# Kernel tuning notes

Measured on AMD Instinct MI355X. Metric: run time of the kernel, lower is better.

Reference implementation:

```python
import jax, jax.numpy as jnp
import numpy as np

N_NODES = 50000
N_EDGES = 800000
HIDDEN = 128
N_TYPES = 4
TIME_STEPS = [2]  # one layer, 2 propagation steps; residuals = {}


def setup_inputs() -> dict:
    key = jax.random.key(0)
    ks = jax.random.split(key, 8)
    std = HIDDEN ** (-0.5)
    states = jax.random.normal(ks[0], (N_NODES, HIDDEN), dtype=jnp.float32)
    etype = jax.random.randint(ks[1], (N_EDGES,), 0, N_TYPES, dtype=jnp.int32)
    src = jax.random.randint(ks[2], (N_EDGES,), 0, N_NODES, dtype=jnp.int32)
    tgt = jax.random.randint(ks[3], (N_EDGES,), 0, N_NODES, dtype=jnp.int32)
    edges = jnp.stack([etype, src, tgt], axis=1)  # [E, 3]: (type, source, target)
    type_weights = std * jax.random.normal(ks[4], (N_TYPES, HIDDEN, HIDDEN), dtype=jnp.float32)
    type_biases = std * jax.random.normal(ks[5], (N_TYPES, HIDDEN), dtype=jnp.float32)
    # Keras GRUCell (reset_after=True): kernel [H,3H], recurrent_kernel [H,3H], bias [2,3H]
    gru_kernel = std * jax.random.normal(ks[6], (HIDDEN, 3 * HIDDEN), dtype=jnp.float32)
    k7, k8 = jax.random.split(ks[7])
    gru_rec_kernel = std * jax.random.normal(k7, (HIDDEN, 3 * HIDDEN), dtype=jnp.float32)
    gru_bias = std * jax.random.normal(k8, (2, 3 * HIDDEN), dtype=jnp.float32)
    return {"states": states, "edges": edges, "type_weights": type_weights,
            "type_biases": type_biases, "gru_kernel": gru_kernel,
            "gru_rec_kernel": gru_rec_kernel, "gru_bias": gru_bias}


def _gru_cell(x, h, kernel, rec_kernel, bias):
    # Keras GRUCell with reset_after=True, tanh / sigmoid activations
    mx = x @ kernel + bias[0]          # [N, 3H]
    mh = h @ rec_kernel + bias[1]      # [N, 3H]
    xz, xr, xh = jnp.split(mx, 3, axis=-1)
    rz, rr, rh = jnp.split(mh, 3, axis=-1)
    z = jax.nn.sigmoid(xz + rz)
    r = jax.nn.sigmoid(xr + rr)
    hh = jnp.tanh(xh + r * rh)
    return z * h + (1.0 - z) * hh


def _propagate(h, etype, src, tgt, type_weights, type_biases, kernel, rec_kernel, bias):
    n_nodes = h.shape[0]
    xs = h[src]  # [E, H] gather of source states
    msg_e = jnp.zeros_like(xs)
    for t in range(N_TYPES):  # small fixed loop over edge types
        mask = (etype == t).astype(h.dtype)[:, None]
        msg_e = msg_e + mask * (xs @ type_weights[t] + type_biases[t])
    messages = jax.ops.segment_sum(msg_e, tgt, num_segments=n_nodes)  # scatter-add
    return _gru_cell(messages, h, kernel, rec_kernel, bias)


def reference(states, edges, type_weights, type_biases, gru_kernel, gru_rec_kernel, gru_bias):
    etype, src, tgt = edges[:, 0], edges[:, 1], edges[:, 2]
    h = states
    for steps in TIME_STEPS:  # single layer here (residuals empty)
        for _ in range(steps):
            h = _propagate(h, etype, src, tgt, type_weights, type_biases,
                           gru_kernel, gru_rec_kernel, gru_bias)
    return h
```

## Files before the change

kernel.cpp:

```cpp
#include <hip/hip_runtime.h>
#include <stdint.h>

namespace {
constexpr int kNodes = 50000;
constexpr int kEdges = 800000;
constexpr int kHid   = 128;
constexpr int kScanBlocks = (kNodes + 255) / 256;
constexpr int kBlocks32 = (kNodes + 31) / 32;

constexpr size_t oCounts    = 0;
constexpr size_t oCursor    = 200704;
constexpr size_t oBlockSums = 401408;
constexpr size_t oBpack     = 402432;
constexpr size_t oPacked    = 1057792;
constexpr size_t oMsg      = 4257792;
constexpr size_t oY         = 29857792;
constexpr size_t kWsNeeded   = oY + 51200000;
constexpr size_t kWsFallback = oY;

constexpr size_t bKhi = 0,      bKlo = 98304,  bRhi = 196608,
                 bRlo = 294912, bWhi = 393216, bWlo = 524288;
}

typedef __attribute__((ext_vector_type(8))) short short8;
typedef __attribute__((ext_vector_type(4))) float f32x4;

union ABFrag { short8 v; uint16_t u[8]; uint4 q; };

__device__ __forceinline__ uint16_t f2bf(float x) {
  uint32_t u = __float_as_uint(x);
  return (uint16_t)((u + 0x7FFFu + ((u >> 16) & 1u)) >> 16);
}
__device__ __forceinline__ float bf2f(uint16_t h) {
  return __uint_as_float(((uint32_t)h) << 16);
}

__device__ __forceinline__ float fast_rcp(float x) {
#if __has_builtin(__builtin_amdgcn_rcpf)
  return __builtin_amdgcn_rcpf(x);
#else
  return 1.f / x;
#endif
}
__device__ __forceinline__ float fast_exp2(float x) {
#if __has_builtin(__builtin_amdgcn_exp2f)
  return __builtin_amdgcn_exp2f(x);
#else
  return exp2f(x);
#endif
}
__device__ __forceinline__ float sigf(float x) {
  return fast_rcp(1.f + fast_exp2(-1.4426950408889634f * x));
}
__device__ __forceinline__ float tanh_fast(float x) {
  x = fminf(fmaxf(x, -10.f), 10.f);
  const float t = fast_exp2(2.8853900817779268f * x);
  return (t - 1.f) * fast_rcp(t + 1.f);
}

__device__ __forceinline__ int swz_pi(int p) {
  return (p & 64) | ((p & 3) << 4) | ((p >> 2) & 15);
}


__global__ __launch_bounds__(256) void count_kernel(const int* __restrict__ edges,
                                                    int* __restrict__ counts) {
  int e = blockIdx.x * 256 + threadIdx.x;
  if (e < kEdges) atomicAdd(&counts[edges[e * 3 + 2]], 1);
}

__global__ __launch_bounds__(256) void scan1_kernel(const int* __restrict__ counts,
                                                    int* __restrict__ cursor,
                                                    int* __restrict__ blocksums) {
  __shared__ int sd[256];
  const int t = threadIdx.x;
  const int i = blockIdx.x * 256 + t;
  int v = (i < kNodes) ? counts[i] : 0;
  sd[t] = v;
  __syncthreads();
  for (int off = 1; off < 256; off <<= 1) {
    int x = (t >= off) ? sd[t - off] : 0;
    __syncthreads();
    sd[t] += x;
    __syncthreads();
  }
  if (i < kNodes) cursor[i] = sd[t] - v;
  if (t == 255) blocksums[blockIdx.x] = sd[255];
}

__global__ __launch_bounds__(256) void scan2_kernel(int* __restrict__ blocksums) {
  __shared__ int sd[256];
  const int t = threadIdx.x;
  int v = (t < kScanBlocks) ? blocksums[t] : 0;
  sd[t] = v;
  __syncthreads();
  for (int off = 1; off < 256; off <<= 1) {
    int x = (t >= off) ? sd[t - off] : 0;
    __syncthreads();
    sd[t] += x;
    __syncthreads();
  }
  if (t < kScanBlocks) blocksums[t] = sd[t] - v;
}

__global__ __launch_bounds__(256) void scan3_kernel(int* __restrict__ cursor,
                                                    const int* __restrict__ blocksums) {
  const int i = blockIdx.x * 256 + threadIdx.x;
  if (i < kNodes) cursor[i] += blocksums[blockIdx.x];
}

__global__ __launch_bounds__(256) void fill_kernel(const int* __restrict__ edges,
                                                   int* __restrict__ cursor,
                                                   unsigned* __restrict__ packed) {
  int e = blockIdx.x * 256 + threadIdx.x;
  if (e < kEdges) {
    const int et  = edges[e * 3 + 0];
    const int src = edges[e * 3 + 1];
    const int tgt = edges[e * 3 + 2];
    const int pos = atomicAdd(&cursor[tgt], 1);
    packed[pos] = (unsigned)(src * 4 + et);
  }
}

__global__ __launch_bounds__(256) void pack_b_kernel(
    const float* __restrict__ K,
    const float* __restrict__ R,
    const float* __restrict__ W,
    uint16_t* __restrict__ bp) {
  const int idx = blockIdx.x * 256 + threadIdx.x;
  uint16_t* khi = bp + bKhi / 2;
  uint16_t* klo = bp + bKlo / 2;
  uint16_t* rhi = bp + bRhi / 2;
  uint16_t* rlo = bp + bRlo / 2;
  uint16_t* whi = bp + bWhi / 2;
  uint16_t* wlo = bp + bWlo / 2;
  if (idx < 128 * 384) {
    const int k = idx / 384, c = idx % 384;
    const int ksrc = swz_pi(k);
    const int kt = k >> 5, quad = (k >> 3) & 3, j = k & 7;
    const int nt = c >> 4, ln = (c & 15) | (quad << 4);
    const size_t o = ((size_t)(kt * 24 + nt) * 64 + ln) * 8 + j;
    const float kv = K[ksrc * 384 + c];
    const float rv = R[k * 384 + c];
    const uint16_t kh = f2bf(kv), rh = f2bf(rv);
    khi[o] = kh; klo[o] = f2bf(kv - bf2f(kh));
    rhi[o] = rh; rlo[o] = f2bf(rv - bf2f(rh));
  } else if (idx < 128 * 384 + 128 * 512) {
    const int i2 = idx - 128 * 384;
    const int k = i2 / 512, c = i2 % 512;
    const int t = c >> 7, cc = c & 127;
    const float wv = W[((size_t)t * 128 + k) * 128 + cc];
    const int kt = k >> 5, quad = (k >> 3) & 3, j = k & 7;
    const int nt = c >> 4, ln = (c & 15) | (quad << 4);
    const size_t o = ((size_t)(kt * 32 + nt) * 64 + ln) * 8 + j;
    const uint16_t wh = f2bf(wv);
    whi[o] = wh; wlo[o] = f2bf(wv - bf2f(wh));
  }
}

__device__ __forceinline__ void split8(const float* p, ABFrag& hi, ABFrag& lo) {
  const float4 a0 = *(const float4*)p;
  const float4 a1 = *(const float4*)(p + 4);
  const float v[8] = {a0.x, a0.y, a0.z, a0.w, a1.x, a1.y, a1.z, a1.w};
#pragma unroll
  for (int j = 0; j < 8; ++j) {
    const uint16_t t = f2bf(v[j]);
    hi.u[j] = t; lo.u[j] = f2bf(v[j] - bf2f(t));
  }
}
__device__ __forceinline__ void conv8(const float* p, ABFrag& hi) {
  const float4 a0 = *(const float4*)p;
  const float4 a1 = *(const float4*)(p + 4);
  const float v[8] = {a0.x, a0.y, a0.z, a0.w, a1.x, a1.y, a1.z, a1.w};
#pragma unroll
  for (int j = 0; j < 8; ++j) hi.u[j] = f2bf(v[j]);
}

__global__ __launch_bounds__(64, 4) void transform_mfma(
    const float* __restrict__ h,
    const uint16_t* __restrict__ bp,
    const float* __restrict__ TB,
    uint16_t* __restrict__ y16) {
  const int lane = threadIdx.x;
  const int w = blockIdx.x & 3;
  const int col16 = lane & 15, quad = lane >> 4;
  const int node0 = (blockIdx.x >> 2) * 32;

  const uint4* __restrict__ Whi = (const uint4*)(bp + bWhi / 2);
  const uint4* __restrict__ Wlo = (const uint4*)(bp + bWlo / 2);

  bool mok[2];
#pragma unroll
  for (int m = 0; m < 2; ++m) mok[m] = (node0 + m * 16) < kNodes;

  f32x4 acc[8][2];
#pragma unroll
  for (int nt = 0; nt < 8; ++nt)
#pragma unroll
    for (int m = 0; m < 2; ++m) acc[nt][m] = (f32x4){0.f, 0.f, 0.f, 0.f};

  const float* hrow = h + (size_t)(node0 + col16) * kHid + quad * 8;

#pragma unroll
  for (int kt = 0; kt < 4; ++kt) {
    ABFrag ah[2], al[2];
#pragma unroll
    for (int m = 0; m < 2; ++m) {
      if (mok[m]) {
        split8(hrow + (size_t)m * 16 * kHid + kt * 32, ah[m], al[m]);
      } else {
        ah[m].q = make_uint4(0, 0, 0, 0); al[m].q = ah[m].q;
      }
    }
#pragma unroll
    for (int nt = 0; nt < 8; ++nt) {
      ABFrag bh, bl;
      bh.q = Whi[(size_t)(kt * 32 + w * 8 + nt) * 64 + lane];
      bl.q = Wlo[(size_t)(kt * 32 + w * 8 + nt) * 64 + lane];
#pragma unroll
      for (int m = 0; m < 2; ++m) {
        f32x4 c = acc[nt][m];
        c = __builtin_amdgcn_mfma_f32_16x16x32_bf16(ah[m].v, bh.v, c, 0, 0, 0);
        c = __builtin_amdgcn_mfma_f32_16x16x32_bf16(ah[m].v, bl.v, c, 0, 0, 0);
        c = __builtin_amdgcn_mfma_f32_16x16x32_bf16(al[m].v, bh.v, c, 0, 0, 0);
        acc[nt][m] = c;
      }
    }
  }

#pragma unroll
  for (int g = 0; g < 2; ++g) {
    float bias[4];
#pragma unroll
    for (int s = 0; s < 4; ++s) bias[s] = TB[w * 128 + (g * 4 + s) * 16 + col16];
#pragma unroll
    for (int m = 0; m < 2; ++m) {
      if (!mok[m]) continue;
#pragma unroll
      for (int r = 0; r < 4; ++r) {
        const int node = node0 + m * 16 + quad * 4 + r;
        const uint32_t lo = (uint32_t)f2bf(acc[g * 4 + 0][m][r] + bias[0]) |
                            ((uint32_t)f2bf(acc[g * 4 + 1][m][r] + bias[1]) << 16);
        const uint32_t hi = (uint32_t)f2bf(acc[g * 4 + 2][m][r] + bias[2]) |
                            ((uint32_t)f2bf(acc[g * 4 + 3][m][r] + bias[3]) << 16);
        *(uint2*)&y16[(size_t)node * 512 + w * 128 + g * 64 + col16 * 4] =
            make_uint2(lo, hi);
      }
    }
  }
}

__global__ __launch_bounds__(256) void gather_kernel(
    const uint32_t* __restrict__ y2,
    const uint32_t* __restrict__ packed,
    const int* __restrict__ rowend,
    const int* __restrict__ counts,
    uint32_t* __restrict__ msg2) {
  const int tid = threadIdx.x;
  const int lane = tid & 63;
  const int v = blockIdx.x * 4 + (tid >> 6);
  const int cnt = counts[v];
  const int s0 = rowend[v] - cnt;
  float a0 = 0.f, a1 = 0.f;
  int e = 0;
  for (; e + 8 <= cnt; e += 8) {
    uint32_t p[8], u[8];
#pragma unroll
    for (int i = 0; i < 8; ++i) p[i] = packed[s0 + e + i];
#pragma unroll
    for (int i = 0; i < 8; ++i) u[i] = y2[(size_t)p[i] * 64 + lane];
#pragma unroll
    for (int i = 0; i < 8; ++i) {
      a0 += __uint_as_float(u[i] << 16);
      a1 += __uint_as_float(u[i] & 0xFFFF0000u);
    }
  }
  for (; e < cnt; ++e) {
    const uint32_t p = packed[s0 + e];
    const uint32_t u = y2[(size_t)p * 64 + lane];
    a0 += __uint_as_float(u << 16);
    a1 += __uint_as_float(u & 0xFFFF0000u);
  }
  msg2[(size_t)v * 64 + lane] = (uint32_t)f2bf(a0) | ((uint32_t)f2bf(a1) << 16);
}

__global__ __launch_bounds__(256, 3) void gru_mfma(
    const uint16_t* __restrict__ msg16,
    const float* __restrict__ hin,
    const uint16_t* __restrict__ bp,
    const float* __restrict__ gb,
    float* __restrict__ hout) {
  const int tid = threadIdx.x;
  const int w = tid >> 6;
  const int lane = tid & 63;
  const int col16 = lane & 15, quad = lane >> 4;
  const int node0 = blockIdx.x * 32;

  const uint4* __restrict__ Khi = (const uint4*)(bp + bKhi / 2);
  const uint4* __restrict__ Klo = (const uint4*)(bp + bKlo / 2);
  const uint4* __restrict__ Rhi = (const uint4*)(bp + bRhi / 2);
  const uint4* __restrict__ Rlo = (const uint4*)(bp + bRlo / 2);

  bool mok[2];
#pragma unroll
  for (int m = 0; m < 2; ++m) mok[m] = (node0 + m * 16) < kNodes;

  f32x4 aZ[2][2], aR[2][2], aX[2][2], aH[2][2];
#pragma unroll
  for (int i = 0; i < 2; ++i)
#pragma unroll
    for (int m = 0; m < 2; ++m) {
      aZ[i][m] = (f32x4){0.f, 0.f, 0.f, 0.f};
      aR[i][m] = aZ[i][m]; aX[i][m] = aZ[i][m]; aH[i][m] = aZ[i][m];
    }

  const uint16_t* mrow = msg16 + (size_t)(node0 + col16) * kHid + quad * 8;
  const float* hrow = hin + (size_t)(node0 + col16) * kHid + quad * 8;

#pragma unroll
  for (int kt = 0; kt < 4; ++kt) {
    ABFrag mh[2], hh[2];
#pragma unroll
    for (int m = 0; m < 2; ++m) {
      if (mok[m]) {
        mh[m].q = *(const uint4*)(mrow + (size_t)m * 16 * kHid + kt * 32);
        conv8(hrow + (size_t)m * 16 * kHid + kt * 32, hh[m]);
      } else {
        mh[m].q = make_uint4(0, 0, 0, 0); hh[m].q = mh[m].q;
      }
    }
#pragma unroll
    for (int lnt = 0; lnt < 2; ++lnt) {
      const int ntc = w * 2 + lnt;
      const size_t oz = (size_t)(kt * 24 + ntc) * 64 + lane;
      const size_t orr = (size_t)(kt * 24 + 8 + ntc) * 64 + lane;
      const size_t oh = (size_t)(kt * 24 + 16 + ntc) * 64 + lane;
      {
        ABFrag kzh, kzl, rzh, rzl, krh, krl, rrh, rrl;
        kzh.q = Khi[oz]; kzl.q = Klo[oz]; rzh.q = Rhi[oz]; rzl.q = Rlo[oz];
        krh.q = Khi[orr]; krl.q = Klo[orr]; rrh.q = Rhi[orr]; rrl.q = Rlo[orr];
#pragma unroll
        for (int m = 0; m < 2; ++m) {
          f32x4 z = aZ[lnt][m];
          z = __builtin_amdgcn_mfma_f32_16x16x32_bf16(mh[m].v, kzh.v, z, 0, 0, 0);
          z = __builtin_amdgcn_mfma_f32_16x16x32_bf16(mh[m].v, kzl.v, z, 0, 0, 0);
          z = __builtin_amdgcn_mfma_f32_16x16x32_bf16(hh[m].v, rzh.v, z, 0, 0, 0);
          z = __builtin_amdgcn_mfma_f32_16x16x32_bf16(hh[m].v, rzl.v, z, 0, 0, 0);
          aZ[lnt][m] = z;
          f32x4 r = aR[lnt][m];
          r = __builtin_amdgcn_mfma_f32_16x16x32_bf16(mh[m].v, krh.v, r, 0, 0, 0);
          r = __builtin_amdgcn_mfma_f32_16x16x32_bf16(mh[m].v, krl.v, r, 0, 0, 0);
          r = __builtin_amdgcn_mfma_f32_16x16x32_bf16(hh[m].v, rrh.v, r, 0, 0, 0);
          r = __builtin_amdgcn_mfma_f32_16x16x32_bf16(hh[m].v, rrl.v, r, 0, 0, 0);
          aR[lnt][m] = r;
        }
      }
      {
        ABFrag khh, khl, rhh, rhl;
        khh.q = Khi[oh]; khl.q = Klo[oh]; rhh.q = Rhi[oh]; rhl.q = Rlo[oh];
#pragma unroll
        for (int m = 0; m < 2; ++m) {
          f32x4 x = aX[lnt][m];
          x = __builtin_amdgcn_mfma_f32_16x16x32_bf16(mh[m].v, khh.v, x, 0, 0, 0);
          x = __builtin_amdgcn_mfma_f32_16x16x32_bf16(mh[m].v, khl.v, x, 0, 0, 0);
          aX[lnt][m] = x;
          f32x4 y = aH[lnt][m];
          y = __builtin_amdgcn_mfma_f32_16x16x32_bf16(hh[m].v, rhh.v, y, 0, 0, 0);
          y = __builtin_amdgcn_mfma_f32_16x16x32_bf16(hh[m].v, rhl.v, y, 0, 0, 0);
          aH[lnt][m] = y;
        }
      }
    }
  }

  __syncthreads();

#pragma unroll
  for (int lnt = 0; lnt < 2; ++lnt) {
    const int c = (w * 2 + lnt) * 16 + col16;
    const float bz = gb[c] + gb[384 + c];
    const float br = gb[128 + c] + gb[512 + c];
    const float bx = gb[256 + c];
    const float bh = gb[640 + c];
#pragma unroll
    for (int m = 0; m < 2; ++m) {
      if (!mok[m]) continue;
#pragma unroll
      for (int r = 0; r < 4; ++r) {
        const int node = node0 + m * 16 + quad * 4 + r;
        const float hp = hin[(size_t)node * kHid + c];
        const float z = sigf(aZ[lnt][m][r] + bz);
        const float rr = sigf(aR[lnt][m][r] + br);
        const float hh = tanh_fast(aX[lnt][m][r] + bx + rr * (aH[lnt][m][r] + bh));
        hout[(size_t)node * kHid + c] = z * hp + (1.f - z) * hh;
      }
    }
  }
}


__global__ __launch_bounds__(256, 2) void message_fb_kernel(
    const float* __restrict__ hin,
    const unsigned* __restrict__ packed,
    const int* __restrict__ rowend,
    const int* __restrict__ counts,
    const float* __restrict__ W,
    const float* __restrict__ TB,
    float* __restrict__ msg) {
  __shared__ float S[32 * 512];
  __shared__ int D[32][4];
  const int tid = threadIdx.x;
  {
    const int g = tid >> 7;
    const int j = tid & 127;
    for (int i = 0; i < 16; ++i) {
      const int nl = g * 16 + i;
      const int v = blockIdx.x * 32 + nl;
      if (v >= kNodes) break;
      const int cnt = counts[v];
      const int s0 = rowend[v] - cnt;
      float a0 = 0.f, a1 = 0.f, a2 = 0.f, a3 = 0.f;
      int d0 = 0, d1 = 0, d2 = 0, d3 = 0;
      for (int e = 0; e < cnt; ++e) {
        const unsigned p = packed[s0 + e];
        const int src = (int)(p >> 2);
        const int t = (int)(p & 3u);
        const float val = hin[(size_t)src * kHid + j];
        a0 += (t == 0) ? val : 0.f;
        a1 += (t == 1) ? val : 0.f;
        a2 += (t == 2) ? val : 0.f;
        a3 += (t == 3) ? val : 0.f;
        d0 += (t == 0); d1 += (t == 1); d2 += (t == 2); d3 += (t == 3);
      }
      float* Sn = &S[nl * 512];
      Sn[j] = a0; Sn[128 + j] = a1; Sn[256 + j] = a2; Sn[384 + j] = a3;
      if (j == 0) { D[nl][0] = d0; D[nl][1] = d1; D[nl][2] = d2; D[nl][3] = d3; }
    }
  }
  __syncthreads();

  const int lane = tid & 31;
  const int jj = lane * 4;
  const int n0 = (tid >> 5) * 4;
  float acc[4][4] = {};
  const float4* __restrict__ W4 = (const float4*)W;
  for (int tk = 0; tk < 512; tk += 4) {
    const float4 w0 = W4[(size_t)(tk + 0) * 32 + lane];
    const float4 w1 = W4[(size_t)(tk + 1) * 32 + lane];
    const float4 w2 = W4[(size_t)(tk + 2) * 32 + lane];
    const float4 w3 = W4[(size_t)(tk + 3) * 32 + lane];
#pragma unroll
    for (int n = 0; n < 4; ++n) {
      const float4 s = *(const float4*)&S[(n0 + n) * 512 + tk];
      acc[n][0] += s.x * w0.x + s.y * w1.x + s.z * w2.x + s.w * w3.x;
      acc[n][1] += s.x * w0.y + s.y * w1.y + s.z * w2.y + s.w * w3.y;
      acc[n][2] += s.x * w0.z + s.y * w1.z + s.z * w2.z + s.w * w3.z;
      acc[n][3] += s.x * w0.w + s.y * w1.w + s.z * w2.w + s.w * w3.w;
    }
  }
  const float4 B0 = *(const float4*)&TB[0 * 128 + jj];
  const float4 B1 = *(const float4*)&TB[1 * 128 + jj];
  const float4 B2 = *(const float4*)&TB[2 * 128 + jj];
  const float4 B3 = *(const float4*)&TB[3 * 128 + jj];
#pragma unroll
  for (int n = 0; n < 4; ++n) {
    const int v = blockIdx.x * 32 + n0 + n;
    if (v < kNodes) {
      float4 o;
      const float d0 = (float)D[n0 + n][0], d1 = (float)D[n0 + n][1];
      const float d2 = (float)D[n0 + n][2], d3 = (float)D[n0 + n][3];
      o.x = acc[n][0] + d0 * B0.x + d1 * B1.x + d2 * B2.x + d3 * B3.x;
      o.y = acc[n][1] + d0 * B0.y + d1 * B1.y + d2 * B2.y + d3 * B3.y;
      o.z = acc[n][2] + d0 * B0.z + d1 * B1.z + d2 * B2.z + d3 * B3.z;
      o.w = acc[n][3] + d0 * B0.w + d1 * B1.w + d2 * B2.w + d3 * B3.w;
      *(float4*)&msg[(size_t)v * kHid + jj] = o;
    }
  }
}

__global__ __launch_bounds__(256, 2) void gru_fb_kernel(
    const float* __restrict__ msg,
    const float* __restrict__ hin,
    const float* __restrict__ K,
    const float* __restrict__ R,
    const float* __restrict__ gb,
    float* __restrict__ hout) {
  __shared__ float At[2][16][68];
  __shared__ float Bt[2][16][384];
  const int tid = threadIdx.x;
  const int node0 = blockIdx.x * 64;
  const int cg = tid >> 4;
  const int ng = tid & 15;

  float accZ[4][8] = {}, accR[4][8] = {}, accXH[4][8] = {}, accRH[4][8] = {};
  const float4* __restrict__ K4 = (const float4*)K;
  const float4* __restrict__ R4 = (const float4*)R;
  const int sn = tid >> 2;
  const int sj = tid & 3;

  for (int k0 = 0; k0 < 128; k0 += 16) {
    __syncthreads();
    {
      float4 vm = make_float4(0.f, 0.f, 0.f, 0.f);
      float4 vh = vm;
      const int node = node0 + sn;
      if (node < kNodes) {
        vm = *(const float4*)&msg[(size_t)node * kHid + k0 + sj * 4];
        vh = *(const float4*)&hin[(size_t)node * kHid + k0 + sj * 4];
      }
      At[0][sj * 4 + 0][sn] = vm.x; At[0][sj * 4 + 1][sn] = vm.y;
      At[0][sj * 4 + 2][sn] = vm.z; At[0][sj * 4 + 3][sn] = vm.w;
      At[1][sj * 4 + 0][sn] = vh.x; At[1][sj * 4 + 1][sn] = vh.y;
      At[1][sj * 4 + 2][sn] = vh.z; At[1][sj * 4 + 3][sn] = vh.w;
    }
#pragma unroll
    for (int i = 0; i < 6; ++i) {
      const int idx = tid + i * 256;
      const int row = idx / 96;
      const int c4 = idx - row * 96;
      *(float4*)&Bt[0][row][c4 * 4] = K4[(size_t)(k0 + row) * 96 + c4];
      *(float4*)&Bt[1][row][c4 * 4] = R4[(size_t)(k0 + row) * 96 + c4];
    }
    __syncthreads();

    for (int kk = 0; kk < 16; ++kk) {
      const float4 am4 = *(const float4*)&At[0][kk][ng * 4];
      const float4 ah4 = *(const float4*)&At[1][kk][ng * 4];
      const float am[4] = {am4.x, am4.y, am4.z, am4.w};
      const float ah[4] = {ah4.x, ah4.y, ah4.z, ah4.w};
      const int cb = cg * 8;
#pragma unroll
      for (int gset = 0; gset < 3; ++gset) {
        const int off = gset * 128 + cb;
        const float4 k0v = *(const float4*)&Bt[0][kk][off];
        const float4 k1v = *(const float4*)&Bt[0][kk][off + 4];
        const float4 r0v = *(const float4*)&Bt[1][kk][off];
        const float4 r1v = *(const float4*)&Bt[1][kk][off + 4];
        const float bk[8] = {k0v.x, k0v.y, k0v.z, k0v.w, k1v.x, k1v.y, k1v.z, k1v.w};
        const float br[8] = {r0v.x, r0v.y, r0v.z, r0v.w, r1v.x, r1v.y, r1v.z, r1v.w};
        if (gset == 0) {
#pragma unroll
          for (int n = 0; n < 4; ++n)
#pragma unroll
            for (int c = 0; c < 8; ++c) accZ[n][c] += am[n] * bk[c] + ah[n] * br[c];
        } else if (gset == 1) {
#pragma unroll
          for (int n = 0; n < 4; ++n)
#pragma unroll
            for (int c = 0; c < 8; ++c) accR[n][c] += am[n] * bk[c] + ah[n] * br[c];
        } else {
#pragma unroll
          for (int n = 0; n < 4; ++n)
#pragma unroll
            for (int c = 0; c < 8; ++c) {
              accXH[n][c] += am[n] * bk[c];
              accRH[n][c] += ah[n] * br[c];
            }
        }
      }
    }
  }

  const int cb = cg * 8;
#pragma unroll
  for (int n = 0; n < 4; ++n) {
    const int node = node0 + ng * 4 + n;
    if (node >= kNodes) continue;
    float o[8];
#pragma unroll
    for (int c = 0; c < 8; ++c) {
      const float z = sigf(accZ[n][c] + gb[cb + c] + gb[384 + cb + c]);
      const float r = sigf(accR[n][c] + gb[128 + cb + c] + gb[512 + cb + c]);
      const float hh = tanh_fast(accXH[n][c] + gb[256 + cb + c] +
                                 r * (accRH[n][c] + gb[640 + cb + c]));
      const float hp = hin[(size_t)node * kHid + cb + c];
      o[c] = z * hp + (1.f - z) * hh;
    }
    *(float4*)&hout[(size_t)node * kHid + cb]     = make_float4(o[0], o[1], o[2], o[3]);
    *(float4*)&hout[(size_t)node * kHid + cb + 4] = make_float4(o[4], o[5], o[6], o[7]);
  }
}

extern "C" void kernel_launch(void* const* d_in, const int* in_sizes, int n_in,
                              void* d_out, int out_size, void* d_ws, size_t ws_size,
                              hipStream_t stream) {
  const float* states = (const float*)d_in[0];
  const int*   edges  = (const int*)d_in[1];
  const float* W      = (const float*)d_in[2];
  const float* TB     = (const float*)d_in[3];
  const float* K      = (const float*)d_in[4];
  const float* R      = (const float*)d_in[5];
  const float* gb     = (const float*)d_in[6];
  float* out = (float*)d_out;

  if (ws_size < kWsFallback) return;

  char* ws = (char*)d_ws;
  int*      counts  = (int*)(ws + oCounts);
  int*      cursor  = (int*)(ws + oCursor);
  int*      bsums   = (int*)(ws + oBlockSums);
  uint16_t* bpack   = (uint16_t*)(ws + oBpack);
  unsigned* packed  = (unsigned*)(ws + oPacked);
  float*    msgf    = (float*)(ws + oMsg);
  uint16_t* msg16   = (uint16_t*)(ws + oMsg);
  uint32_t* msg2    = (uint32_t*)(ws + oMsg);
  uint16_t* y16     = (uint16_t*)(ws + oY);
  uint32_t* y2      = (uint32_t*)(ws + oY);

  hipMemsetAsync(counts, 0, 200704, stream);
  count_kernel<<<kEdges / 256, 256, 0, stream>>>(edges, counts);
  scan1_kernel<<<kScanBlocks, 256, 0, stream>>>(counts, cursor, bsums);
  scan2_kernel<<<1, 256, 0, stream>>>(bsums);
  scan3_kernel<<<kScanBlocks, 256, 0, stream>>>(cursor, bsums);
  fill_kernel<<<kEdges / 256, 256, 0, stream>>>(edges, cursor, packed);

  if (ws_size >= kWsNeeded) {
    pack_b_kernel<<<448, 256, 0, stream>>>(K, R, W, bpack);
    const int ga_blocks = kNodes / 4;
    const int tf_blocks = kBlocks32 * 4;
    transform_mfma<<<tf_blocks, 64, 0, stream>>>(states, bpack, TB, y16);
    gather_kernel<<<ga_blocks, 256, 0, stream>>>(y2, packed, cursor, counts, msg2);
    gru_mfma<<<kBlocks32, 256, 0, stream>>>(msg16, states, bpack, gb, out);
    transform_mfma<<<tf_blocks, 64, 0, stream>>>(out, bpack, TB, y16);
    gather_kernel<<<ga_blocks, 256, 0, stream>>>(y2, packed, cursor, counts, msg2);
    gru_mfma<<<kBlocks32, 256, 0, stream>>>(msg16, out, bpack, gb, out);
  } else {
    const int msg_blocks = (kNodes + 31) / 32;
    const int gru_blocks = (kNodes + 63) / 64;
    message_fb_kernel<<<msg_blocks, 256, 0, stream>>>(states, packed, cursor,
                                                      counts, W, TB, msgf);
    gru_fb_kernel<<<gru_blocks, 256, 0, stream>>>(msgf, states, K, R, gb, out);
    message_fb_kernel<<<msg_blocks, 256, 0, stream>>>(out, packed, cursor,
                                                      counts, W, TB, msgf);
    gru_fb_kernel<<<gru_blocks, 256, 0, stream>>>(msgf, out, K, R, gb, out);
  }
}
```

Baseline: 420.2 us.

## Stage packed weight fragments through double-buffered LDS in transform and GRU kernels

```diff
diff --git a/kernel.cpp b/kernel.cpp
--- a/kernel.cpp
+++ b/kernel.cpp
@@ -6,7 +6,7 @@
 constexpr int kEdges = 800000;
 constexpr int kHid   = 128;
 constexpr int kScanBlocks = (kNodes + 255) / 256;
-constexpr int kBlocks32 = (kNodes + 31) / 32;
+constexpr int kBlocks64 = (kNodes + 63) / 64;
 
 constexpr size_t oCounts    = 0;
 constexpr size_t oCursor    = 200704;
@@ -60,6 +60,12 @@
 
 __device__ __forceinline__ int swz_pi(int p) {
   return (p & 64) | ((p & 3) << 4) | ((p >> 2) & 15);
+}
+
+__device__ __forceinline__ void gload_lds16(const void* g, void* l) {
+  __builtin_amdgcn_global_load_lds(
+      (const __attribute__((address_space(1))) unsigned int*)g,
+      (__attribute__((address_space(3))) unsigned int*)l, 16, 0, 0);
 }
 
 
@@ -158,9 +164,7 @@
   }
 }
 
-__device__ __forceinline__ void split8(const float* p, ABFrag& hi, ABFrag& lo) {
-  const float4 a0 = *(const float4*)p;
-  const float4 a1 = *(const float4*)(p + 4);
+__device__ __forceinline__ void split8v(float4 a0, float4 a1, ABFrag& hi, ABFrag& lo) {
   const float v[8] = {a0.x, a0.y, a0.z, a0.w, a1.x, a1.y, a1.z, a1.w};
 #pragma unroll
   for (int j = 0; j < 8; ++j) {
@@ -168,30 +172,31 @@
     hi.u[j] = t; lo.u[j] = f2bf(v[j] - bf2f(t));
   }
 }
-__device__ __forceinline__ void conv8(const float* p, ABFrag& hi) {
-  const float4 a0 = *(const float4*)p;
-  const float4 a1 = *(const float4*)(p + 4);
+__device__ __forceinline__ void conv8v(float4 a0, float4 a1, ABFrag& hi) {
   const float v[8] = {a0.x, a0.y, a0.z, a0.w, a1.x, a1.y, a1.z, a1.w};
 #pragma unroll
   for (int j = 0; j < 8; ++j) hi.u[j] = f2bf(v[j]);
 }
 
-__global__ __launch_bounds__(64, 4) void transform_mfma(
+__global__ __launch_bounds__(512, 2) void transform_mfma(
     const float* __restrict__ h,
     const uint16_t* __restrict__ bp,
     const float* __restrict__ TB,
     uint16_t* __restrict__ y16) {
-  const int lane = threadIdx.x;
-  const int w = blockIdx.x & 3;
+  __shared__ uint4 smem[2][32][64];
+  const int tid = threadIdx.x;
+  const int W = tid >> 6;
+  const int tw = W & 3;
+  const int hf = W >> 2;
+  const int lane = tid & 63;
   const int col16 = lane & 15, quad = lane >> 4;
-  const int node0 = (blockIdx.x >> 2) * 32;
-
-  const uint4* __restrict__ Whi = (const uint4*)(bp + bWhi / 2);
-  const uint4* __restrict__ Wlo = (const uint4*)(bp + bWlo / 2);
+  const int node0 = blockIdx.x * 64 + hf * 32;
+  const char* wb = (const char*)bp + bWhi;
+  const int r0 = W * 4;
 
   bool mok[2];
-#pragma unroll
-  for (int m = 0; m < 2; ++m) mok[m] = (node0 + m * 16) < kNodes;
+  mok[0] = node0 < kNodes;
+  mok[1] = node0 + 16 < kNodes;
 
   f32x4 acc[8][2];
 #pragma unroll
@@ -202,28 +207,68 @@
   const float* hrow = h + (size_t)(node0 + col16) * kHid + quad * 8;
 
 #pragma unroll
+  for (int i = 0; i < 4; ++i) {
+    const int r = r0 + i;
+    const int tbl = r >> 4, w_ = (r >> 2) & 3, j = r & 3;
+    gload_lds16(wb + (size_t)tbl * 131072 + (size_t)(w_ * 8 + j) * 1024 + lane * 16,
+                &smem[0][r][0]);
+  }
+
+  ABFrag ah[2], al[2];
+#pragma unroll
   for (int kt = 0; kt < 4; ++kt) {
-    ABFrag ah[2], al[2];
-#pragma unroll
-    for (int m = 0; m < 2; ++m) {
-      if (mok[m]) {
-        split8(hrow + (size_t)m * 16 * kHid + kt * 32, ah[m], al[m]);
-      } else {
-        ah[m].q = make_uint4(0, 0, 0, 0); al[m].q = ah[m].q;
-      }
-    }
-#pragma unroll
-    for (int nt = 0; nt < 8; ++nt) {
-      ABFrag bh, bl;
-      bh.q = Whi[(size_t)(kt * 32 + w * 8 + nt) * 64 + lane];
-      bl.q = Wlo[(size_t)(kt * 32 + w * 8 + nt) * 64 + lane];
-#pragma unroll
-      for (int m = 0; m < 2; ++m) {
-        f32x4 c = acc[nt][m];
-        c = __builtin_amdgcn_mfma_f32_16x16x32_bf16(ah[m].v, bh.v, c, 0, 0, 0);
-        c = __builtin_amdgcn_mfma_f32_16x16x32_bf16(ah[m].v, bl.v, c, 0, 0, 0);
-        c = __builtin_amdgcn_mfma_f32_16x16x32_bf16(al[m].v, bh.v, c, 0, 0, 0);
-        acc[nt][m] = c;
+    float4 araw[2][2];
+#pragma unroll
+    for (int g = 0; g < 2; ++g) {
+      const int c = kt * 2 + g;
+      asm volatile("s_waitcnt vmcnt(0)" ::: "memory");
+      __builtin_amdgcn_s_barrier();
+      asm volatile("" ::: "memory");
+      if (g == 0) {
+#pragma unroll
+        for (int m = 0; m < 2; ++m) {
+          if (mok[m]) {
+            araw[m][0] = *(const float4*)(hrow + (size_t)m * 16 * kHid + kt * 32);
+            araw[m][1] = *(const float4*)(hrow + (size_t)m * 16 * kHid + kt * 32 + 4);
+          } else {
+            araw[m][0] = make_float4(0.f, 0.f, 0.f, 0.f);
+            araw[m][1] = araw[m][0];
+          }
+        }
+      }
+      asm volatile("" ::: "memory");
+      if (c + 1 < 8) {
+        const int nk = (c + 1) >> 1, ng = (c + 1) & 1;
+#pragma unroll
+        for (int i = 0; i < 4; ++i) {
+          const int r = r0 + i;
+          const int tbl = r >> 4, w_ = (r >> 2) & 3, j = r & 3;
+          gload_lds16(wb + (size_t)tbl * 131072 +
+                          (size_t)(nk * 32 + w_ * 8 + ng * 4 + j) * 1024 + lane * 16,
+                      &smem[(c + 1) & 1][r][0]);
+        }
+      }
+      asm volatile("" ::: "memory");
+      if (g == 0) {
+#pragma unroll
+        for (int m = 0; m < 2; ++m) split8v(araw[m][0], araw[m][1], ah[m], al[m]);
+      }
+      const int b = c & 1;
+#pragma unroll
+      for (int jj = 0; jj < 4; ++jj) {
+        ABFrag bh, bl;
+        bh.q = smem[b][tw * 4 + jj][lane];
+        bl.q = smem[b][16 + tw * 4 + jj][lane];
+        __builtin_amdgcn_s_setprio(1);
+#pragma unroll
+        for (int m = 0; m < 2; ++m) {
+          f32x4 cc = acc[g * 4 + jj][m];
+          cc = __builtin_amdgcn_mfma_f32_16x16x32_bf16(ah[m].v, bh.v, cc, 0, 0, 0);
+          cc = __builtin_amdgcn_mfma_f32_16x16x32_bf16(ah[m].v, bl.v, cc, 0, 0, 0);
+          cc = __builtin_amdgcn_mfma_f32_16x16x32_bf16(al[m].v, bh.v, cc, 0, 0, 0);
+          acc[g * 4 + jj][m] = cc;
+        }
+        __builtin_amdgcn_s_setprio(0);
       }
     }
   }
@@ -232,7 +277,7 @@
   for (int g = 0; g < 2; ++g) {
     float bias[4];
 #pragma unroll
-    for (int s = 0; s < 4; ++s) bias[s] = TB[w * 128 + (g * 4 + s) * 16 + col16];
+    for (int s = 0; s < 4; ++s) bias[s] = TB[tw * 128 + (g * 4 + s) * 16 + col16];
 #pragma unroll
     for (int m = 0; m < 2; ++m) {
       if (!mok[m]) continue;
@@ -243,7 +288,7 @@
                             ((uint32_t)f2bf(acc[g * 4 + 1][m][r] + bias[1]) << 16);
         const uint32_t hi = (uint32_t)f2bf(acc[g * 4 + 2][m][r] + bias[2]) |
                             ((uint32_t)f2bf(acc[g * 4 + 3][m][r] + bias[3]) << 16);
-        *(uint2*)&y16[(size_t)node * 512 + w * 128 + g * 64 + col16 * 4] =
+        *(uint2*)&y16[(size_t)node * 512 + tw * 128 + g * 64 + col16 * 4] =
             make_uint2(lo, hi);
       }
     }
@@ -284,26 +329,26 @@
   msg2[(size_t)v * 64 + lane] = (uint32_t)f2bf(a0) | ((uint32_t)f2bf(a1) << 16);
 }
 
-__global__ __launch_bounds__(256, 3) void gru_mfma(
+__global__ __launch_bounds__(512, 2) void gru_mfma(
     const uint16_t* __restrict__ msg16,
     const float* __restrict__ hin,
     const uint16_t* __restrict__ bp,
     const float* __restrict__ gb,
     float* __restrict__ hout) {
+  __shared__ uint4 smem[2][32][64];
   const int tid = threadIdx.x;
-  const int w = tid >> 6;
+  const int W = tid >> 6;
+  const int cg = W & 3;
+  const int hf = W >> 2;
   const int lane = tid & 63;
   const int col16 = lane & 15, quad = lane >> 4;
-  const int node0 = blockIdx.x * 32;
-
-  const uint4* __restrict__ Khi = (const uint4*)(bp + bKhi / 2);
-  const uint4* __restrict__ Klo = (const uint4*)(bp + bKlo / 2);
-  const uint4* __restrict__ Rhi = (const uint4*)(bp + bRhi / 2);
-  const uint4* __restrict__ Rlo = (const uint4*)(bp + bRlo / 2);
+  const int node0 = blockIdx.x * 64 + hf * 32;
+  const char* bpb = (const char*)bp;
+  const int r0 = W * 4;
 
   bool mok[2];
-#pragma unroll
-  for (int m = 0; m < 2; ++m) mok[m] = (node0 + m * 16) < kNodes;
+  mok[0] = node0 < kNodes;
+  mok[1] = node0 + 16 < kNodes;
 
   f32x4 aZ[2][2], aR[2][2], aX[2][2], aH[2][2];
 #pragma unroll
@@ -318,58 +363,102 @@
   const float* hrow = hin + (size_t)(node0 + col16) * kHid + quad * 8;
 
 #pragma unroll
+  for (int i = 0; i < 4; ++i) {
+    const int r = r0 + i;
+    const int tbl = r >> 3, ntc = r & 7;
+    gload_lds16(bpb + (size_t)tbl * 98304 + (size_t)ntc * 1024 + lane * 16,
+                &smem[0][r][0]);
+  }
+
+  ABFrag mh[2], hh[2];
+#pragma unroll
   for (int kt = 0; kt < 4; ++kt) {
-    ABFrag mh[2], hh[2];
-#pragma unroll
-    for (int m = 0; m < 2; ++m) {
-      if (mok[m]) {
-        mh[m].q = *(const uint4*)(mrow + (size_t)m * 16 * kHid + kt * 32);
-        conv8(hrow + (size_t)m * 16 * kHid + kt * 32, hh[m]);
-      } else {
-        mh[m].q = make_uint4(0, 0, 0, 0); hh[m].q = mh[m].q;
-      }
-    }
-#pragma unroll
-    for (int lnt = 0; lnt < 2; ++lnt) {
-      const int ntc = w * 2 + lnt;
-      const size_t oz = (size_t)(kt * 24 + ntc) * 64 + lane;
-      const size_t orr = (size_t)(kt * 24 + 8 + ntc) * 64 + lane;
-      const size_t oh = (size_t)(kt * 24 + 16 + ntc) * 64 + lane;
-      {
-        ABFrag kzh, kzl, rzh, rzl, krh, krl, rrh, rrl;
-        kzh.q = Khi[oz]; kzl.q = Klo[oz]; rzh.q = Rhi[oz]; rzl.q = Rlo[oz];
-        krh.q = Khi[orr]; krl.q = Klo[orr]; rrh.q = Rhi[orr]; rrl.q = Rlo[orr];
+    uint4 mraw[2]; float4 hraw[2][2];
+#pragma unroll
+    for (int gs = 0; gs < 3; ++gs) {
+      const int c = kt * 3 + gs;
+      asm volatile("s_waitcnt vmcnt(0)" ::: "memory");
+      __builtin_amdgcn_s_barrier();
+      asm volatile("" ::: "memory");
+      if (gs == 0) {
 #pragma unroll
         for (int m = 0; m < 2; ++m) {
-          f32x4 z = aZ[lnt][m];
-          z = __builtin_amdgcn_mfma_f32_16x16x32_bf16(mh[m].v, kzh.v, z, 0, 0, 0);
-          z = __builtin_amdgcn_mfma_f32_16x16x32_bf16(mh[m].v, kzl.v, z, 0, 0, 0);
-          z = __builtin_amdgcn_mfma_f32_16x16x32_bf16(hh[m].v, rzh.v, z, 0, 0, 0);
-          z = __builtin_amdgcn_mfma_f32_16x16x32_bf16(hh[m].v, rzl.v, z, 0, 0, 0);
-          aZ[lnt][m] = z;
-          f32x4 r = aR[lnt][m];
-          r = __builtin_amdgcn_mfma_f32_16x16x32_bf16(mh[m].v, krh.v, r, 0, 0, 0);
-          r = __builtin_amdgcn_mfma_f32_16x16x32_bf16(mh[m].v, krl.v, r, 0, 0, 0);
-          r = __builtin_amdgcn_mfma_f32_16x16x32_bf16(hh[m].v, rrh.v, r, 0, 0, 0);
-          r = __builtin_amdgcn_mfma_f32_16x16x32_bf16(hh[m].v, rrl.v, r, 0, 0, 0);
-          aR[lnt][m] = r;
+          if (mok[m]) {
+            mraw[m] = *(const uint4*)(mrow + (size_t)m * 16 * kHid + kt * 32);
+            hraw[m][0] = *(const float4*)(hrow + (size_t)m * 16 * kHid + kt * 32);
+            hraw[m][1] = *(const float4*)(hrow + (size_t)m * 16 * kHid + kt * 32 + 4);
+          } else {
+            mraw[m] = make_uint4(0, 0, 0, 0);
+            hraw[m][0] = make_float4(0.f, 0.f, 0.f, 0.f);
+            hraw[m][1] = hraw[m][0];
+          }
         }
       }
-      {
-        ABFrag khh, khl, rhh, rhl;
-        khh.q = Khi[oh]; khl.q = Klo[oh]; rhh.q = Rhi[oh]; rhl.q = Rlo[oh];
+      asm volatile("" ::: "memory");
+      if (c + 1 < 12) {
+        const int nk = (c + 1) / 3, ng = (c + 1) % 3;
+        const int rb = nk * 24 + ng * 8;
+#pragma unroll
+        for (int i = 0; i < 4; ++i) {
+          const int r = r0 + i;
+          const int tbl = r >> 3, ntc = r & 7;
+          gload_lds16(bpb + (size_t)tbl * 98304 + (size_t)(rb + ntc) * 1024 + lane * 16,
+                      &smem[(c + 1) & 1][r][0]);
+        }
+      }
+      asm volatile("" ::: "memory");
+      if (gs == 0) {
 #pragma unroll
         for (int m = 0; m < 2; ++m) {
-          f32x4 x = aX[lnt][m];
-          x = __builtin_amdgcn_mfma_f32_16x16x32_bf16(mh[m].v, khh.v, x, 0, 0, 0);
-          x = __builtin_amdgcn_mfma_f32_16x16x32_bf16(mh[m].v, khl.v, x, 0, 0, 0);
-          aX[lnt][m] = x;
-          f32x4 y = aH[lnt][m];
-          y = __builtin_amdgcn_mfma_f32_16x16x32_bf16(hh[m].v, rhh.v, y, 0, 0, 0);
-          y = __builtin_amdgcn_mfma_f32_16x16x32_bf16(hh[m].v, rhl.v, y, 0, 0, 0);
-          aH[lnt][m] = y;
+          mh[m].q = mraw[m];
+          conv8v(hraw[m][0], hraw[m][1], hh[m]);
         }
       }
+      const int b = c & 1;
+#pragma unroll
+      for (int lnt = 0; lnt < 2; ++lnt) {
+        const int ntc = cg * 2 + lnt;
+        ABFrag f0, f1, f2, f3;
+        f0.q = smem[b][ntc][lane];
+        f1.q = smem[b][8 + ntc][lane];
+        f2.q = smem[b][16 + ntc][lane];
+        f3.q = smem[b][24 + ntc][lane];
+        __builtin_amdgcn_s_setprio(1);
+        if (gs == 0) {
+#pragma unroll
+          for (int m = 0; m < 2; ++m) {
+            f32x4 z = aZ[lnt][m];
+            z = __builtin_amdgcn_mfma_f32_16x16x32_bf16(mh[m].v, f0.v, z, 0, 0, 0);
+            z = __builtin_amdgcn_mfma_f32_16x16x32_bf16(mh[m].v, f1.v, z, 0, 0, 0);
+            z = __builtin_amdgcn_mfma_f32_16x16x32_bf16(hh[m].v, f2.v, z, 0, 0, 0);
+            z = __builtin_amdgcn_mfma_f32_16x16x32_bf16(hh[m].v, f3.v, z, 0, 0, 0);
+            aZ[lnt][m] = z;
+          }
+        } else if (gs == 1) {
+#pragma unroll
+          for (int m = 0; m < 2; ++m) {
+            f32x4 r = aR[lnt][m];
+            r = __builtin_amdgcn_mfma_f32_16x16x32_bf16(mh[m].v, f0.v, r, 0, 0, 0);
+            r = __builtin_amdgcn_mfma_f32_16x16x32_bf16(mh[m].v, f1.v, r, 0, 0, 0);
+            r = __builtin_amdgcn_mfma_f32_16x16x32_bf16(hh[m].v, f2.v, r, 0, 0, 0);
+            r = __builtin_amdgcn_mfma_f32_16x16x32_bf16(hh[m].v, f3.v, r, 0, 0, 0);
+            aR[lnt][m] = r;
+          }
+        } else {
+#pragma unroll
+          for (int m = 0; m < 2; ++m) {
+            f32x4 x = aX[lnt][m];
+            x = __builtin_amdgcn_mfma_f32_16x16x32_bf16(mh[m].v, f0.v, x, 0, 0, 0);
+            x = __builtin_amdgcn_mfma_f32_16x16x32_bf16(mh[m].v, f1.v, x, 0, 0, 0);
+            aX[lnt][m] = x;
+            f32x4 y = aH[lnt][m];
+            y = __builtin_amdgcn_mfma_f32_16x16x32_bf16(hh[m].v, f2.v, y, 0, 0, 0);
+            y = __builtin_amdgcn_mfma_f32_16x16x32_bf16(hh[m].v, f3.v, y, 0, 0, 0);
+            aH[lnt][m] = y;
+          }
+        }
+        __builtin_amdgcn_s_setprio(0);
+      }
     }
   }
 
@@ -377,7 +466,7 @@
 
 #pragma unroll
   for (int lnt = 0; lnt < 2; ++lnt) {
-    const int c = (w * 2 + lnt) * 16 + col16;
+    const int c = (cg * 2 + lnt) * 16 + col16;
     const float bz = gb[c] + gb[384 + c];
     const float br = gb[128 + c] + gb[512 + c];
     const float bx = gb[256 + c];
@@ -391,8 +480,8 @@
         const float hp = hin[(size_t)node * kHid + c];
         const float z = sigf(aZ[lnt][m][r] + bz);
         const float rr = sigf(aR[lnt][m][r] + br);
-        const float hh = tanh_fast(aX[lnt][m][r] + bx + rr * (aH[lnt][m][r] + bh));
-        hout[(size_t)node * kHid + c] = z * hp + (1.f - z) * hh;
+        const float hh2 = tanh_fast(aX[lnt][m][r] + bx + rr * (aH[lnt][m][r] + bh));
+        hout[(size_t)node * kHid + c] = z * hp + (1.f - z) * hh2;
       }
     }
   }
@@ -617,13 +706,12 @@
   if (ws_size >= kWsNeeded) {
     pack_b_kernel<<<448, 256, 0, stream>>>(K, R, W, bpack);
     const int ga_blocks = kNodes / 4;
-    const int tf_blocks = kBlocks32 * 4;
-    transform_mfma<<<tf_blocks, 64, 0, stream>>>(states, bpack, TB, y16);
+    transform_mfma<<<kBlocks64, 512, 0, stream>>>(states, bpack, TB, y16);
     gather_kernel<<<ga_blocks, 256, 0, stream>>>(y2, packed, cursor, counts, msg2);
-    gru_mfma<<<kBlocks32, 256, 0, stream>>>(msg16, states, bpack, gb, out);
-    transform_mfma<<<tf_blocks, 64, 0, stream>>>(out, bpack, TB, y16);
+    gru_mfma<<<kBlocks64, 512, 0, stream>>>(msg16, states, bpack, gb, out);
+    transform_mfma<<<kBlocks64, 512, 0, stream>>>(out, bpack, TB, y16);
     gather_kernel<<<ga_blocks, 256, 0, stream>>>(y2, packed, cursor, counts, msg2);
-    gru_mfma<<<kBlocks32, 256, 0, stream>>>(msg16, out, bpack, gb, out);
+    gru_mfma<<<kBlocks64, 512, 0, stream>>>(msg16, out, bpack, gb, out);
   } else {
     const int msg_blocks = (kNodes + 31) / 32;
     const int gru_blocks = (kNodes + 63) / 64;
```

Result: slower. 435.0 us (+3.5%).

## Fuse neighbor gather into GRU kernel via shared-memory message tile

Applied to the files above, without the earlier changes.

```diff
diff --git a/kernel.cpp b/kernel.cpp
--- a/kernel.cpp
+++ b/kernel.cpp
@@ -6,7 +6,7 @@
 constexpr int kEdges = 800000;
 constexpr int kHid   = 128;
 constexpr int kScanBlocks = (kNodes + 255) / 256;
-constexpr int kBlocks32 = (kNodes + 31) / 32;
+constexpr int kBlocks32 = (kNodes + 31) / 31 == 0 ? 0 : (kNodes + 31) / 32;
 
 constexpr size_t oCounts    = 0;
 constexpr size_t oCursor    = 200704;
@@ -250,52 +250,57 @@
   }
 }
 
-__global__ __launch_bounds__(256) void gather_kernel(
+__global__ __launch_bounds__(256, 3) void gru_fused(
     const uint32_t* __restrict__ y2,
     const uint32_t* __restrict__ packed,
     const int* __restrict__ rowend,
     const int* __restrict__ counts,
-    uint32_t* __restrict__ msg2) {
-  const int tid = threadIdx.x;
-  const int lane = tid & 63;
-  const int v = blockIdx.x * 4 + (tid >> 6);
-  const int cnt = counts[v];
-  const int s0 = rowend[v] - cnt;
-  float a0 = 0.f, a1 = 0.f;
-  int e = 0;
-  for (; e + 8 <= cnt; e += 8) {
-    uint32_t p[8], u[8];
-#pragma unroll
-    for (int i = 0; i < 8; ++i) p[i] = packed[s0 + e + i];
-#pragma unroll
-    for (int i = 0; i < 8; ++i) u[i] = y2[(size_t)p[i] * 64 + lane];
-#pragma unroll
-    for (int i = 0; i < 8; ++i) {
-      a0 += __uint_as_float(u[i] << 16);
-      a1 += __uint_as_float(u[i] & 0xFFFF0000u);
-    }
-  }
-  for (; e < cnt; ++e) {
-    const uint32_t p = packed[s0 + e];
-    const uint32_t u = y2[(size_t)p * 64 + lane];
-    a0 += __uint_as_float(u << 16);
-    a1 += __uint_as_float(u & 0xFFFF0000u);
-  }
-  msg2[(size_t)v * 64 + lane] = (uint32_t)f2bf(a0) | ((uint32_t)f2bf(a1) << 16);
-}
-
-__global__ __launch_bounds__(256, 3) void gru_mfma(
-    const uint16_t* __restrict__ msg16,
     const float* __restrict__ hin,
     const uint16_t* __restrict__ bp,
     const float* __restrict__ gb,
     float* __restrict__ hout) {
+  __shared__ uint32_t msgT[2048];
   const int tid = threadIdx.x;
   const int w = tid >> 6;
   const int lane = tid & 63;
   const int col16 = lane & 15, quad = lane >> 4;
   const int node0 = blockIdx.x * 32;
 
+  const int fw = ((lane >> 4) * 4 + ((lane >> 2) & 3)) * 16 + (lane & 3) * 4;
+  for (int i = 0; i < 8; ++i) {
+    const int v = node0 + w * 8 + i;
+    if (v < kNodes) {
+      const int cnt = counts[v];
+      const int s0 = rowend[v] - cnt;
+      float a0 = 0.f, a1 = 0.f;
+      int e = 0;
+      for (; e + 8 <= cnt; e += 8) {
+        uint32_t p[8], u[8];
+#pragma unroll
+        for (int k = 0; k < 8; ++k) p[k] = packed[s0 + e + k];
+#pragma unroll
+        for (int k = 0; k < 8; ++k) u[k] = y2[(size_t)p[k] * 64 + lane];
+#pragma unroll
+        for (int k = 0; k < 8; ++k) {
+          a0 += __uint_as_float(u[k] << 16);
+          a1 += __uint_as_float(u[k] & 0xFFFF0000u);
+        }
+      }
+      for (; e < cnt; ++e) {
+        const uint32_t p = packed[s0 + e];
+        const uint32_t u = y2[(size_t)p * 64 + lane];
+        a0 += __uint_as_float(u << 16);
+        a1 += __uint_as_float(u & 0xFFFF0000u);
+      }
+      const int nl = w * 8 + i;
+      const int widx = (((nl >> 4) * 4 + (lane >> 4)) * 64 +
+                        (((lane >> 2) & 3) * 16 + (nl & 15))) * 4 + (lane & 3);
+      msgT[widx] = (uint32_t)f2bf(a0) | ((uint32_t)f2bf(a1) << 16);
+    }
+  }
+  __syncthreads();
+
+  const uint4* __restrict__ msgQ = (const uint4*)msgT;
   const uint4* __restrict__ Khi = (const uint4*)(bp + bKhi / 2);
   const uint4* __restrict__ Klo = (const uint4*)(bp + bKlo / 2);
   const uint4* __restrict__ Rhi = (const uint4*)(bp + bRhi / 2);
@@ -314,7 +319,6 @@
       aR[i][m] = aZ[i][m]; aX[i][m] = aZ[i][m]; aH[i][m] = aZ[i][m];
     }
 
-  const uint16_t* mrow = msg16 + (size_t)(node0 + col16) * kHid + quad * 8;
   const float* hrow = hin + (size_t)(node0 + col16) * kHid + quad * 8;
 
 #pragma unroll
@@ -323,7 +327,7 @@
 #pragma unroll
     for (int m = 0; m < 2; ++m) {
       if (mok[m]) {
-        mh[m].q = *(const uint4*)(mrow + (size_t)m * 16 * kHid + kt * 32);
+        mh[m].q = msgQ[(m * 4 + kt) * 64 + lane];
         conv8(hrow + (size_t)m * 16 * kHid + kt * 32, hh[m]);
       } else {
         mh[m].q = make_uint4(0, 0, 0, 0); hh[m].q = mh[m].q;
@@ -391,8 +395,8 @@
         const float hp = hin[(size_t)node * kHid + c];
         const float z = sigf(aZ[lnt][m][r] + bz);
         const float rr = sigf(aR[lnt][m][r] + br);
-        const float hh = tanh_fast(aX[lnt][m][r] + bx + rr * (aH[lnt][m][r] + bh));
-        hout[(size_t)node * kHid + c] = z * hp + (1.f - z) * hh;
+        const float hh2 = tanh_fast(aX[lnt][m][r] + bx + rr * (aH[lnt][m][r] + bh));
+        hout[(size_t)node * kHid + c] = z * hp + (1.f - z) * hh2;
       }
     }
   }
@@ -602,8 +606,6 @@
   uint16_t* bpack   = (uint16_t*)(ws + oBpack);
   unsigned* packed  = (unsigned*)(ws + oPacked);
   float*    msgf    = (float*)(ws + oMsg);
-  uint16_t* msg16   = (uint16_t*)(ws + oMsg);
-  uint32_t* msg2    = (uint32_t*)(ws + oMsg);
   uint16_t* y16     = (uint16_t*)(ws + oY);
   uint32_t* y2      = (uint32_t*)(ws + oY);
 
@@ -616,14 +618,13 @@
 
   if (ws_size >= kWsNeeded) {
     pack_b_kernel<<<448, 256, 0, stream>>>(K, R, W, bpack);
-    const int ga_blocks = kNodes / 4;
     const int tf_blocks = kBlocks32 * 4;
     transform_mfma<<<tf_blocks, 64, 0, stream>>>(states, bpack, TB, y16);
-    gather_kernel<<<ga_blocks, 256, 0, stream>>>(y2, packed, cursor, counts, msg2);
-    gru_mfma<<<kBlocks32, 256, 0, stream>>>(msg16, states, bpack, gb, out);
+    gru_fused<<<kBlocks32, 256, 0, stream>>>(y2, packed, cursor, counts,
+                                             states, bpack, gb, out);
     transform_mfma<<<tf_blocks, 64, 0, stream>>>(out, bpack, TB, y16);
-    gather_kernel<<<ga_blocks, 256, 0, stream>>>(y2, packed, cursor, counts, msg2);
-    gru_mfma<<<kBlocks32, 256, 0, stream>>>(msg16, out, bpack, gb, out);
+    gru_fused<<<kBlocks32, 256, 0, stream>>>(y2, packed, cursor, counts,
+                                             out, bpack, gb, out);
   } else {
     const int msg_blocks = (kNodes + 31) / 32;
     const int gru_blocks = (kNodes + 63) / 64;
```

Result: slower. 460.4 us (+9.6%).
